# Performance work log

Measured on AMD Instinct MI355X. Metric: run time of the kernel, lower is better.

The kernel has to match this reference:

```python
import jax, jax.numpy as jnp
import numpy as np

DIM = 128; D_STATE = 16; D_CONV = 4; EXPAND = 2
D_INNER = DIM * EXPAND            # 256
DT_RANK = (DIM + 15) // 16        # 8
B, H, W = 2, 56, 56


def _ln(x, w, b):
    m = jnp.mean(x, -1, keepdims=True)
    v = jnp.var(x, -1, keepdims=True)
    return (x - m) * jax.lax.rsqrt(v + 1e-5) * w + b


def _mamba(x, in_w, conv_w, conv_b, xproj_w, dt_w, dt_b, A_log, Dp, out_w):
    # x: (B, L, DIM)
    Bb, L, _ = x.shape
    xz = x @ in_w.T                                   # (B,L,2*D_INNER)
    xi, z = jnp.split(xz, 2, axis=-1)
    # causal depthwise conv1d (pad left d_conv-1, truncate to L)
    xc = jnp.transpose(xi, (0, 2, 1))                 # (B,D_INNER,L)
    xc = jax.lax.conv_general_dilated(
        xc, conv_w, (1,), [(D_CONV - 1, 0)],
        dimension_numbers=('NCH', 'OIH', 'NCH'),
        feature_group_count=D_INNER) + conv_b[None, :, None]
    xs = jax.nn.silu(jnp.transpose(xc, (0, 2, 1)))    # (B,L,D_INNER)
    dbl = xs @ xproj_w.T                              # (B,L,DT_RANK+2*D_STATE)
    dt = jax.nn.softplus(dbl[..., :DT_RANK] @ dt_w.T + dt_b)   # (B,L,D_INNER)
    Bc = dbl[..., DT_RANK:DT_RANK + D_STATE]          # (B,L,D_STATE)
    Cc = dbl[..., DT_RANK + D_STATE:]                 # (B,L,D_STATE)
    A = -jnp.exp(A_log)                               # (D_INNER,D_STATE)
    dA = jnp.exp(dt[..., None] * A)                   # (B,L,D_INNER,D_STATE)
    dBu = (dt * xs)[..., None] * Bc[:, :, None, :]    # (B,L,D_INNER,D_STATE)

    def step(h, inp):
        a, bu, c = inp
        h = a * h + bu                                # (B,D_INNER,D_STATE)
        return h, jnp.einsum('bdn,bn->bd', h, c)

    h0 = jnp.zeros((Bb, D_INNER, D_STATE), x.dtype)
    _, ys = jax.lax.scan(step, h0, (jnp.moveaxis(dA, 1, 0),
                                    jnp.moveaxis(dBu, 1, 0),
                                    jnp.moveaxis(Cc, 1, 0)))
    y = jnp.moveaxis(ys, 0, 1) + xs * Dp              # (B,L,D_INNER)
    y = y * jax.nn.silu(z)
    return y @ out_w.T                                # (B,L,DIM)


def _forward(x, norm_h_w, norm_h_b, norm_v_w, norm_v_b,
             dw_w, dw_b, pw_w, pw_b,
             h_in_w, h_conv_w, h_conv_b, h_xproj_w, h_dt_w, h_dt_b, h_A_log, h_D, h_out_w,
             v_in_w, v_conv_w, v_conv_b, v_xproj_w, v_dt_w, v_dt_b, v_A_log, v_D, v_out_w,
             ca_fc1_w, ca_fc2_w):
    Bb, C, Hh, Ww = x.shape
    # local branch: depthwise 3x3 + GELU + 1x1
    lf = jax.lax.conv_general_dilated(
        x, dw_w, (1, 1), [(1, 1), (1, 1)],
        dimension_numbers=('NCHW', 'OIHW', 'NCHW'),
        feature_group_count=C) + dw_b[None, :, None, None]
    lf = jax.nn.gelu(lf, approximate=False)
    lf = jnp.einsum('bchw,oc->bohw', lf, pw_w[:, :, 0, 0]) + pw_b[None, :, None, None]
    # horizontal scan: row-major tokens
    xh = _ln(x.reshape(Bb, C, Hh * Ww).transpose(0, 2, 1), norm_h_w, norm_h_b)
    oh = _mamba(xh, h_in_w, h_conv_w, h_conv_b, h_xproj_w, h_dt_w, h_dt_b,
                h_A_log, h_D, h_out_w)
    oh = oh.transpose(0, 2, 1).reshape(Bb, C, Hh, Ww)
    # vertical scan: column-major tokens
    xv = _ln(jnp.transpose(x, (0, 1, 3, 2)).reshape(Bb, C, Ww * Hh).transpose(0, 2, 1),
             norm_v_w, norm_v_b)
    ov = _mamba(xv, v_in_w, v_conv_w, v_conv_b, v_xproj_w, v_dt_w, v_dt_b,
                v_A_log, v_D, v_out_w)
    ov = jnp.transpose(ov.transpose(0, 2, 1).reshape(Bb, C, Ww, Hh), (0, 1, 3, 2))
    fused = oh + ov + lf
    # channel attention
    y = jnp.mean(fused, axis=(2, 3))                  # (B,C)
    y = jax.nn.sigmoid(jax.nn.relu(y @ ca_fc1_w.T) @ ca_fc2_w.T)
    return fused * y[:, :, None, None] + x


def setup_inputs() -> dict:
    key = jax.random.key(0)
    ks = iter(jax.random.split(key, 64))
    def nrm(shape, scale):
        return jax.random.normal(next(ks), shape, jnp.float32) * scale
    d = {}
    d['x'] = nrm((B, DIM, H, W), 1.0)
    d['norm_h_w'] = jnp.ones((DIM,), jnp.float32); d['norm_h_b'] = jnp.zeros((DIM,), jnp.float32)
    d['norm_v_w'] = jnp.ones((DIM,), jnp.float32); d['norm_v_b'] = jnp.zeros((DIM,), jnp.float32)
    d['dw_w'] = nrm((DIM, 1, 3, 3), 1.0 / 3.0)
    d['dw_b'] = jnp.zeros((DIM,), jnp.float32)
    d['pw_w'] = nrm((DIM, DIM, 1, 1), DIM ** -0.5)
    d['pw_b'] = jnp.zeros((DIM,), jnp.float32)
    for p in ('h', 'v'):
        d[p + '_in_w'] = nrm((2 * D_INNER, DIM), DIM ** -0.5)
        d[p + '_conv_w'] = nrm((D_INNER, 1, D_CONV), D_CONV ** -0.5)
        d[p + '_conv_b'] = jnp.zeros((D_INNER,), jnp.float32)
        d[p + '_xproj_w'] = nrm((DT_RANK + 2 * D_STATE, D_INNER), D_INNER ** -0.5)
        d[p + '_dt_w'] = nrm((D_INNER, DT_RANK), DT_RANK ** -0.5)
        d[p + '_dt_b'] = jnp.full((D_INNER,), -2.0, jnp.float32)  # small positive dt
        d[p + '_A_log'] = jnp.log(jnp.tile(jnp.arange(1, D_STATE + 1, dtype=jnp.float32), (D_INNER, 1)))
        d[p + '_D'] = jnp.ones((D_INNER,), jnp.float32)
        d[p + '_out_w'] = nrm((DIM, D_INNER), D_INNER ** -0.5)
    d['ca_fc1_w'] = nrm((DIM // 4, DIM), DIM ** -0.5)
    d['ca_fc2_w'] = nrm((DIM, DIM // 4), (DIM // 4) ** -0.5)
    return d


def reference(x, norm_h_w, norm_h_b, norm_v_w, norm_v_b,
              dw_w, dw_b, pw_w, pw_b,
              h_in_w, h_conv_w, h_conv_b, h_xproj_w, h_dt_w, h_dt_b, h_A_log, h_D, h_out_w,
              v_in_w, v_conv_w, v_conv_b, v_xproj_w, v_dt_w, v_dt_b, v_A_log, v_D, v_out_w,
              ca_fc1_w, ca_fc2_w):
    return _forward(x, norm_h_w, norm_h_b, norm_v_w, norm_v_b,
                    dw_w, dw_b, pw_w, pw_b,
                    h_in_w, h_conv_w, h_conv_b, h_xproj_w, h_dt_w, h_dt_b, h_A_log, h_D, h_out_w,
                    v_in_w, v_conv_w, v_conv_b, v_xproj_w, v_dt_w, v_dt_b, v_A_log, v_D, v_out_w,
                    ca_fc1_w, ca_fc2_w)
```

## Files before the change

kernel.cpp:

```cpp
#include <hip/hip_runtime.h>
#include <hip/hip_bf16.h>

typedef __hip_bfloat16 bf16;
__device__ __forceinline__ float b2f(bf16 v){ return __bfloat162float(v); }
__device__ __forceinline__ bf16 f2b(float v){ return __float2bfloat16(v); }

typedef __attribute__((ext_vector_type(8))) short frag_ab;
typedef __attribute__((ext_vector_type(4))) float frag_cd;
typedef __attribute__((ext_vector_type(4))) short short4v;

__device__ __forceinline__ frag_ab ld_frag_2xb64(const bf16* p){
  union { frag_ab f; short4v h[2]; } u;
  u.h[0] = *reinterpret_cast<const short4v*>(p);
  u.h[1] = *reinterpret_cast<const short4v*>(p+4);
  return u.f;
}

__device__ __forceinline__ void st_agent(float* p, float v){
  __hip_atomic_store(p, v, __ATOMIC_RELAXED, __HIP_MEMORY_SCOPE_AGENT);
}
__device__ __forceinline__ float ld_agent(const float* p){
  return __hip_atomic_load(p, __ATOMIC_RELAXED, __HIP_MEMORY_SCOPE_AGENT);
}

#define LLEN 3136
#define BATCH 2
#define NCHUNK 49
#define LC 64

__global__ void k_front(const float* __restrict__ x, const float* __restrict__ dww,
                        const float* __restrict__ dwb, bf16* __restrict__ tmp,
                        const float* nhw_, const float* nhb_, const float* nvw_,
                        const float* nvb_, bf16* __restrict__ xln,
                        float* __restrict__ YMEAN, int* __restrict__ ZCNT){
  int blk = blockIdx.x;
  int tid = threadIdx.x;
  if (blk < 1024){
    int bc = blk & 255;
    int seg = blk >> 8;
    int c = bc & 127;
    if (blk == 0){
      if (tid < 256) YMEAN[tid] = 0.f;
      if (tid < 4)   ZCNT[tid] = 0;
    }
    const float* xp = x + (size_t)bc*LLEN;
    float w[9];
    #pragma unroll
    for (int i=0;i<9;i++) w[i] = dww[c*9+i];
    float bias = dwb[c];
    int pstart = seg * 784;
    for (int p = pstart + tid; p < pstart + 784; p += 256){
      int i = p/56, j = p%56;
      float acc = bias;
      #pragma unroll
      for (int a=0;a<3;a++){
        int ii = i + a - 1;
        if (ii < 0 || ii >= 56) continue;
        #pragma unroll
        for (int bb=0;bb<3;bb++){
          int jj = j + bb - 1;
          if (jj < 0 || jj >= 56) continue;
          acc += w[a*3+bb] * xp[ii*56+jj];
        }
      }
      float g = 0.5f*acc*(1.0f + erff(acc*0.70710678118654752f));
      tmp[(size_t)bc*LLEN + p] = f2b(g);
    }
  } else {
    int idx2 = blk - 1024;
    int h = idx2 % 56, b = idx2 / 56;
    __shared__ float sx[128][57];
    __shared__ float smean[56], srstd[56];
    __shared__ float wh[128], bh[128], wv_[128], bv_[128];
    if (tid < 128){ wh[tid]=nhw_[tid]; bh[tid]=nhb_[tid];
                    wv_[tid]=nvw_[tid]; bv_[tid]=nvb_[tid]; }
    for (int idx = tid; idx < 128*56; idx += 256){
      int c = idx / 56, w = idx % 56;
      sx[c][w] = x[((size_t)(b*128+c))*LLEN + h*56 + w];
    }
    __syncthreads();
    if (tid < 56){
      float s=0.f, s2=0.f;
      for (int c=0;c<128;c++){ float v = sx[c][tid]; s+=v; s2+=v*v; }
      float m = s*(1.f/128.f);
      float var = s2*(1.f/128.f) - m*m;
      smean[tid]=m; srstd[tid]=rsqrtf(var+1e-5f);
    }
    __syncthreads();
    bf16* outh = xln;
    bf16* outv = xln + (size_t)BATCH*LLEN*128;
    for (int idx = tid; idx < 56*128; idx += 256){
      int w = idx >> 7, c = idx & 127;
      float v = (sx[c][w]-smean[w])*srstd[w];
      outh[((size_t)b*LLEN + h*56 + w)*128 + c] = f2b(v*wh[c]+bh[c]);
      outv[((size_t)b*LLEN + w*56 + h)*128 + c] = f2b(v*wv_[c]+bv_[c]);
    }
  }
}

__global__ void k_inproj(const bf16* __restrict__ xln, const float* __restrict__ hw,
                         const float* __restrict__ vw, bf16* __restrict__ XI, bf16* __restrict__ Z){
  int dir = blockIdx.z;
  const bf16* A = xln + (size_t)dir*BATCH*LLEN*128;
  const float* W = dir ? vw : hw;
  int m0 = blockIdx.x*64;
  int npair = blockIdx.y*128;
  __shared__ __align__(16) bf16 sA[64][136];
  __shared__ __align__(16) bf16 sW[64][136];
  int tid = threadIdx.x;
  #pragma unroll
  for (int r=0;r<4;r++){
    int idx = tid + r*256;
    int row = idx >> 4, c8 = (idx & 15)*8;
    *reinterpret_cast<float4*>(&sA[row][c8]) =
        *reinterpret_cast<const float4*>(&A[(size_t)(m0+row)*128 + c8]);
  }
  int wv2 = tid >> 6, lane = tid & 63;
  int qd = lane >> 4, mr = lane & 15;
  bf16* dst = (npair < 256) ? XI : Z;
  int nbase0 = npair & 255;
  size_t dslab = (size_t)dir*BATCH*LLEN*256;
  #pragma unroll
  for (int nt=0; nt<2; nt++){
    int n0 = npair + nt*64;
    __syncthreads();
    #pragma unroll
    for (int r=0;r<8;r++){
      int idx = tid + r*256;
      int row = idx >> 5, c4 = (idx & 31)*4;
      float4 w4 = *reinterpret_cast<const float4*>(&W[(size_t)(n0+row)*128 + c4]);
      bf16 t4[4] = {f2b(w4.x), f2b(w4.y), f2b(w4.z), f2b(w4.w)};
      *reinterpret_cast<double*>(&sW[row][c4]) = *reinterpret_cast<double*>(t4);
    }
    __syncthreads();
    frag_cd acc[4] = {};
    #pragma unroll
    for (int k0=0;k0<128;k0+=32){
      frag_ab af = *reinterpret_cast<frag_ab*>(&sA[wv2*16+mr][k0+qd*8]);
      #pragma unroll
      for (int t=0;t<4;t++){
        frag_ab bfr = *reinterpret_cast<frag_ab*>(&sW[t*16+mr][k0+qd*8]);
        acc[t] = __builtin_amdgcn_mfma_f32_16x16x32_bf16(af, bfr, acc[t], 0, 0, 0);
      }
    }
    int nb = nbase0 + nt*64;
    #pragma unroll
    for (int t=0;t<4;t++)
      #pragma unroll
      for (int r=0;r<4;r++){
        int row = m0 + wv2*16 + qd*4 + r;
        int col = nb + t*16 + mr;
        dst[dslab + (size_t)row*256 + col] = f2b(acc[t][r]);
      }
  }
}

__global__ void k_dbl(const bf16* __restrict__ XI,
                      const float* hcw, const float* hcb, const float* vcw, const float* vcb,
                      const float* __restrict__ hx, const float* __restrict__ vx,
                      const float* hdw, const float* vdw, const float* hdb, const float* vdb,
                      bf16* __restrict__ XS2, bf16* __restrict__ DT2,
                      float* __restrict__ Bf, float* __restrict__ Cf){
  int m0 = blockIdx.x*64;
  int bd = m0 / LLEN;
  int l0m = m0 % LLEN;
  int dirq = bd >> 1;
  const bf16* XId = XI + (size_t)bd*LLEN*256;
  const float* W = dirq ? vx : hx;
  const float* cw = dirq ? vcw : hcw;
  const float* cb = dirq ? vcb : hcb;
  __shared__ __align__(16) bf16 sA[67][264];
  __shared__ __align__(16) bf16 sW[48][264];
  __shared__ float sdbl[64][49];
  int tid = threadIdx.x;
  for (int idx = tid; idx < 67*32; idx += 256){
    int row = idx >> 5, c8 = (idx & 31)*8;
    int l = l0m - 3 + row;
    float4 v = make_float4(0.f,0.f,0.f,0.f);
    if (l >= 0) v = *reinterpret_cast<const float4*>(&XId[(size_t)l*256 + c8]);
    *reinterpret_cast<float4*>(&sA[row][c8]) = v;
  }
  #pragma unroll
  for (int r=0;r<12;r++){
    int idx = tid + r*256;
    int row = idx >> 6, c4 = (idx & 63)*4;
    bf16 t4[4] = {f2b(0.f), f2b(0.f), f2b(0.f), f2b(0.f)};
    if (row < 40){
      float4 w4 = *reinterpret_cast<const float4*>(&W[(size_t)row*256 + c4]);
      t4[0]=f2b(w4.x); t4[1]=f2b(w4.y); t4[2]=f2b(w4.z); t4[3]=f2b(w4.w);
    }
    *reinterpret_cast<double*>(&sW[row][c4]) = *reinterpret_cast<double*>(t4);
  }
  __syncthreads();
  {
    float w0=cw[tid*4], w1=cw[tid*4+1], w2=cw[tid*4+2], w3=cw[tid*4+3];
    float cbias = cb[tid];
    size_t x2base = ((size_t)bd*16 + (tid>>4))*LLEN + l0m;
    int c16 = tid & 15;
    float xm3 = b2f(sA[0][tid]), xm2 = b2f(sA[1][tid]), xm1 = b2f(sA[2][tid]);
    #pragma unroll 4
    for (int j=0;j<64;j++){
      float x0 = b2f(sA[j+3][tid]);
      float acc = cbias + w0*xm3 + w1*xm2 + w2*xm1 + w3*x0;
      float s = acc / (1.f + __expf(-acc));
      bf16 sv = f2b(s);
      sA[j][tid] = sv;
      XS2[(x2base + j)*16 + c16] = sv;
      xm3=xm2; xm2=xm1; xm1=x0;
    }
  }
  __syncthreads();
  int wv2 = tid >> 6, lane = tid & 63;
  int qd = lane >> 4, mr = lane & 15;
  frag_cd acc[3] = {};
  #pragma unroll
  for (int k0=0;k0<256;k0+=32){
    frag_ab af = *reinterpret_cast<frag_ab*>(&sA[wv2*16+mr][k0+qd*8]);
    #pragma unroll
    for (int t=0;t<3;t++){
      frag_ab bfr = *reinterpret_cast<frag_ab*>(&sW[t*16+mr][k0+qd*8]);
      acc[t] = __builtin_amdgcn_mfma_f32_16x16x32_bf16(af, bfr, acc[t], 0, 0, 0);
    }
  }
  #pragma unroll
  for (int t=0;t<3;t++)
    #pragma unroll
    for (int r=0;r<4;r++){
      int col = t*16 + mr;
      if (col < 40) sdbl[wv2*16 + qd*4 + r][col] = acc[t][r];
    }
  __syncthreads();
  const float* dtw = dirq ? vdw : hdw;
  const float* dtb = dirq ? vdb : hdb;
  float w8[8];
  #pragma unroll
  for (int r=0;r<8;r++) w8[r] = dtw[tid*8+r];
  float biasv = dtb[tid];
  size_t d2base = ((size_t)bd*16 + (tid>>4))*LLEN + l0m;
  int c16 = tid & 15;
  for (int row=0; row<64; row++){
    float a = biasv;
    #pragma unroll
    for (int r=0;r<8;r++) a += sdbl[row][r]*w8[r];
    float sv = (a > 20.f) ? a : __logf(1.f + __expf(a));
    DT2[(d2base + row)*16 + c16] = f2b(sv);
  }
  #pragma unroll
  for (int r=0;r<8;r++){
    int idx = tid + r*256;
    int row = idx >> 5, o = idx & 31;
    float v = sdbl[row][8+o];
    size_t rr = (size_t)(m0+row)*16;
    if (o < 16) Bf[rr + o] = v;
    else        Cf[rr + (o-16)] = v;
  }
}

__global__ void k_scan1(const bf16* __restrict__ DT2, const bf16* __restrict__ XS2,
                        const float* __restrict__ Bc, const float* hA, const float* vA,
                        float* __restrict__ Pbuf, float* __restrict__ Hbuf){
  int bd = blockIdx.z;
  int g  = blockIdx.y;
  int ck = blockIdx.x;
  int l0 = ck*LC;
  const float* Bd = Bc + (size_t)bd*LLEN*16;
  const float* Alog = (bd >> 1) ? vA : hA;
  int tid = threadIdx.x;
  int dl = tid >> 4, n = tid & 15;
  float A = -__expf(Alog[(g*16+dl)*16+n]);
  __shared__ float sdt[LC][16], sxs[LC][16], sB[LC][16];
  size_t base2 = (((size_t)bd*16 + g)*LLEN + l0)*16;
  #pragma unroll
  for (int r=0;r<4;r++){
    int idx = tid + r*256;
    sdt[idx>>4][idx&15] = b2f(DT2[base2 + idx]);
    sxs[idx>>4][idx&15] = b2f(XS2[base2 + idx]);
    (&sB[0][0])[idx] = Bd[(size_t)l0*16 + idx];
  }
  __syncthreads();
  float h = 0.f, P = 1.f;
  #pragma unroll 8
  for (int i=0;i<LC;i++){
    float a = sdt[i][dl];
    float u = sxs[i][dl];
    float dA = __expf(a * A);
    h = dA*h + (a*u)*sB[i][n];
    P *= dA;
  }
  size_t sidx = (((size_t)bd*16 + g)*NCHUNK + ck)*256 + tid;
  Pbuf[sidx] = P;
  Hbuf[sidx] = h;
}

__global__ void k_scan2(const float* __restrict__ Pbuf, float* __restrict__ Hbuf){
  int q = blockIdx.x;
  int tid = threadIdx.x;
  size_t qb = (size_t)q*NCHUNK*256 + tid;
  float Pv[7], Hv[7];
  float carry = 0.f;
  #pragma unroll
  for (int j=0;j<7;j++){
    Pv[j] = Pbuf[qb + (size_t)j*256];
    Hv[j] = Hbuf[qb + (size_t)j*256];
  }
  #pragma unroll
  for (int b=0;b<7;b++){
    float Pn[7], Hn[7];
    if (b < 6){
      #pragma unroll
      for (int j=0;j<7;j++){
        Pn[j] = Pbuf[qb + (size_t)((b+1)*7+j)*256];
        Hn[j] = Hbuf[qb + (size_t)((b+1)*7+j)*256];
      }
    }
    #pragma unroll
    for (int j=0;j<7;j++){
      Hbuf[qb + (size_t)(b*7+j)*256] = carry;
      carry = Pv[j]*carry + Hv[j];
    }
    if (b < 6){
      #pragma unroll
      for (int j=0;j<7;j++){ Pv[j] = Pn[j]; Hv[j] = Hn[j]; }
    }
  }
}

__global__ void k_scan3(const bf16* __restrict__ DT2, const bf16* __restrict__ XS2,
                        const float* __restrict__ Bc, const float* __restrict__ Cc,
                        const float* hA, const float* vA,
                        const float* __restrict__ Hbuf, bf16* __restrict__ ys){
  int bd = blockIdx.z;
  int g  = blockIdx.y;
  int ck = blockIdx.x;
  int l0 = ck*LC;
  const float* Bd = Bc + (size_t)bd*LLEN*16;
  const float* Cd = Cc + (size_t)bd*LLEN*16;
  bf16* yd = ys + (size_t)bd*LLEN*256;
  const float* Alog = (bd >> 1) ? vA : hA;
  int tid = threadIdx.x;
  int dl = tid >> 4, n = tid & 15;
  float A = -__expf(Alog[(g*16+dl)*16+n]);
  __shared__ float sdt[LC][16], sxs[LC][16], sB[LC][16], sC[LC][16];
  __shared__ float sp2[16][272];
  size_t base2 = (((size_t)bd*16 + g)*LLEN + l0)*16;
  #pragma unroll
  for (int r=0;r<4;r++){
    int idx = tid + r*256;
    sdt[idx>>4][idx&15] = b2f(DT2[base2 + idx]);
    sxs[idx>>4][idx&15] = b2f(XS2[base2 + idx]);
    (&sB[0][0])[idx] = Bd[(size_t)l0*16 + idx];
    (&sC[0][0])[idx] = Cd[(size_t)l0*16 + idx];
  }
  size_t sidx = (((size_t)bd*16 + g)*NCHUNK + ck)*256 + tid;
  float h = Hbuf[sidx];
  __syncthreads();
  int swz = dl*17 + n;
  int i_local = tid >> 4;
  int c16 = tid & 15;
  int rbase = c16*17;
  for (int i0=0; i0<LC; i0+=16){
    #pragma unroll
    for (int ii=0;ii<16;ii++){
      int i = i0 + ii;
      float a = sdt[i][dl];
      float u = sxs[i][dl];
      float dA = __expf(a * A);
      h = dA*h + (a*u)*sB[i][n];
      sp2[ii][swz] = h * sC[i][n];
    }
    __syncthreads();
    const float* row = &sp2[i_local][rbase];
    float s = 0.f;
    #pragma unroll
    for (int k=0;k<16;k++) s += row[k];
    yd[(size_t)(l0+i0+i_local)*256 + g*16 + c16] = f2b(s);
    __syncthreads();
  }
}

__global__ void k_outgemm(const bf16* __restrict__ ys, const bf16* __restrict__ XS2,
                          const bf16* __restrict__ Z, const float* __restrict__ hD,
                          const float* __restrict__ vD, const float* __restrict__ how,
                          const float* __restrict__ vow, bf16* __restrict__ OD){
  int dir = blockIdx.y;
  size_t slab = (size_t)dir*BATCH*LLEN*256;
  const float* W = dir ? vow : how;
  const float* Dw = dir ? vD : hD;
  bf16* od = OD + (size_t)dir*BATCH*LLEN*128;
  int m0 = blockIdx.x*32;
  int bd = dir*2 + m0/LLEN;
  int lbase = m0 % LLEN;
  __shared__ __align__(16) bf16 sA[32][264];
  __shared__ __align__(16) bf16 sW[64][264];
  int tid = threadIdx.x;
  #pragma unroll
  for (int r=0;r<4;r++){
    int idx = tid + r*256;
    int row = idx >> 5, c8 = (idx & 31)*8;
    size_t e = slab + (size_t)(m0+row)*256 + c8;
    size_t e2 = (((size_t)bd*16 + (c8>>4))*LLEN + lbase + row)*16 + (c8&15);
    bf16 yb[8], xb[8], zb[8], ob[8];
    *reinterpret_cast<float4*>(yb) = *reinterpret_cast<const float4*>(&ys[e]);
    *reinterpret_cast<float4*>(xb) = *reinterpret_cast<const float4*>(&XS2[e2]);
    *reinterpret_cast<float4*>(zb) = *reinterpret_cast<const float4*>(&Z[e]);
    #pragma unroll
    for (int j=0;j<8;j++){
      float Dv = Dw[c8 + j];
      float yv = b2f(yb[j]) + b2f(xb[j])*Dv;
      float zv = b2f(zb[j]);
      ob[j] = f2b(yv * (zv/(1.f+__expf(-zv))));
    }
    *reinterpret_cast<float4*>(&sA[row][c8]) = *reinterpret_cast<float4*>(ob);
  }
  int wv2 = tid >> 6, lane = tid & 63;
  int qd = lane >> 4, mr = lane & 15;
  int msub = wv2 & 1, tpair = (wv2 >> 1)*2;
  #pragma unroll
  for (int nh=0; nh<2; nh++){
    int n0 = nh*64;
    __syncthreads();
    #pragma unroll
    for (int r=0;r<16;r++){
      int idx = tid + r*256;
      int row = idx >> 6, c4 = (idx & 63)*4;
      float4 w4 = *reinterpret_cast<const float4*>(&W[(size_t)(n0+row)*256 + c4]);
      bf16 t4[4] = {f2b(w4.x), f2b(w4.y), f2b(w4.z), f2b(w4.w)};
      *reinterpret_cast<double*>(&sW[row][c4]) = *reinterpret_cast<double*>(t4);
    }
    __syncthreads();
    frag_cd acc[2] = {};
    #pragma unroll
    for (int k0=0;k0<256;k0+=32){
      frag_ab af = *reinterpret_cast<frag_ab*>(&sA[msub*16+mr][k0+qd*8]);
      #pragma unroll
      for (int i=0;i<2;i++){
        frag_ab bfr = *reinterpret_cast<frag_ab*>(&sW[(tpair+i)*16+mr][k0+qd*8]);
        acc[i] = __builtin_amdgcn_mfma_f32_16x16x32_bf16(af, bfr, acc[i], 0, 0, 0);
      }
    }
    #pragma unroll
    for (int i=0;i<2;i++)
      #pragma unroll
      for (int r=0;r<4;r++){
        int row = m0 + msub*16 + qd*4 + r;
        int col = n0 + (tpair+i)*16 + mr;
        od[(size_t)row*128 + col] = f2b(acc[i][r]);
      }
  }
}

__global__ void k_pwcomb(const bf16* __restrict__ tmp, const float* __restrict__ pww,
                         const float* __restrict__ pwb, const bf16* __restrict__ OD,
                         const float* __restrict__ x, float* __restrict__ out,
                         float* __restrict__ YMEAN, int* __restrict__ CNTPW,
                         int* __restrict__ FLAG, float* __restrict__ GATE,
                         const float* __restrict__ fc1, const float* __restrict__ fc2){
  int p0 = blockIdx.x * 64;
  int m0 = blockIdx.y * 64;
  int b  = blockIdx.z;
  const bf16* T = tmp + (size_t)b*128*LLEN;
  const bf16* od0 = OD + (size_t)b*LLEN*128;
  const bf16* od1 = OD + (size_t)(BATCH + b)*LLEN*128;
  __shared__ __align__(16) bf16 sA[64][136];
  __shared__ __align__(16) bf16 sBt[64][132];
  __shared__ float sOD[64][65];
  __shared__ float ym[128], s1g[32];
  __shared__ int slast;
  int tid = threadIdx.x;
  #pragma unroll
  for (int r=0;r<8;r++){
    int idx = tid + r*256;
    int row = idx >> 5, c4 = (idx & 31)*4;
    float4 w4 = *reinterpret_cast<const float4*>(&pww[(size_t)(m0+row)*128 + c4]);
    bf16 t4[4] = {f2b(w4.x), f2b(w4.y), f2b(w4.z), f2b(w4.w)};
    *reinterpret_cast<double*>(&sA[row][c4]) = *reinterpret_cast<double*>(t4);
  }
  #pragma unroll
  for (int r=0;r<8;r++){
    int idx = tid + r*256;
    int c = idx >> 4, p4 = (idx & 15)*4;
    union { double d; bf16 v[4]; } u;
    u.d = *reinterpret_cast<const double*>(&T[(size_t)c*LLEN + p0 + p4]);
    #pragma unroll
    for (int j=0;j<4;j++) sBt[p4+j][c] = u.v[j];
  }
  #pragma unroll
  for (int r=0;r<8;r++){
    int idx = tid + r*256;
    int prow = idx >> 5, mp = (idx & 31)*2;
    int p = p0 + prow;
    int pi = p/56, pj = p%56;
    int pt = pj*56 + pi;
    bf16 a0[2], a1[2];
    *reinterpret_cast<float*>(a0) = *reinterpret_cast<const float*>(&od0[(size_t)p*128 + m0 + mp]);
    *reinterpret_cast<float*>(a1) = *reinterpret_cast<const float*>(&od1[(size_t)pt*128 + m0 + mp]);
    sOD[prow][mp]   = b2f(a0[0]) + b2f(a1[0]);
    sOD[prow][mp+1] = b2f(a0[1]) + b2f(a1[1]);
  }
  __syncthreads();
  int wv2 = tid >> 6, lane = tid & 63;
  int qd = lane >> 4, mr = lane & 15;
  frag_cd acc[4] = {};
  #pragma unroll
  for (int k0=0;k0<128;k0+=32){
    frag_ab af = *reinterpret_cast<frag_ab*>(&sA[wv2*16+mr][k0+qd*8]);
    #pragma unroll
    for (int t=0;t<4;t++){
      frag_ab bfr = ld_frag_2xb64(&sBt[t*16+mr][k0+qd*8]);
      acc[t] = __builtin_amdgcn_mfma_f32_16x16x32_bf16(af, bfr, acc[t], 0, 0, 0);
    }
  }
  float vals[4][4];
  #pragma unroll
  for (int r=0;r<4;r++){
    int m = m0 + wv2*16 + qd*4 + r;
    float bias = pwb[m];
    float s = 0.f;
    #pragma unroll
    for (int t=0;t<4;t++){
      float val = acc[t][r] + bias + sOD[t*16+mr][m - m0];
      vals[t][r] = val;
      s += val;
    }
    s += __shfl_xor(s, 1, 16);
    s += __shfl_xor(s, 2, 16);
    s += __shfl_xor(s, 4, 16);
    s += __shfl_xor(s, 8, 16);
    if (mr == 0) atomicAdd(&YMEAN[b*128 + m], s);
  }
  __syncthreads();
  if (tid == 0) slast = (atomicAdd(&CNTPW[b], 1) == 2*49 - 1);
  __syncthreads();
  if (slast){
    if (tid < 128)
      ym[tid] = ld_agent(&YMEAN[b*128+tid]) * (1.f/(float)LLEN);
    __syncthreads();
    {
      int o = tid >> 3, part = tid & 7;
      float a = 0.f;
      #pragma unroll
      for (int k=0;k<16;k++) a += ym[part*16 + k] * fc1[o*128 + part*16 + k];
      a += __shfl_xor(a, 1, 8);
      a += __shfl_xor(a, 2, 8);
      a += __shfl_xor(a, 4, 8);
      if (part == 0) s1g[o] = fmaxf(a, 0.f);
    }
    __syncthreads();
    if (tid < 128){
      float a = 0.f;
      #pragma unroll
      for (int j=0;j<32;j++) a += s1g[j]*fc2[tid*32+j];
      st_agent(&GATE[b*128+tid], 1.f/(1.f+__expf(-a)));
    }
    __syncthreads();
    if (tid == 0)
      __hip_atomic_store(&FLAG[b], 1, __ATOMIC_RELEASE, __HIP_MEMORY_SCOPE_AGENT);
  } else {
    if (tid == 0)
      while (__hip_atomic_load(&FLAG[b], __ATOMIC_ACQUIRE, __HIP_MEMORY_SCOPE_AGENT) == 0)
        __builtin_amdgcn_s_sleep(2);
  }
  __syncthreads();
  float g4[4];
  #pragma unroll
  for (int r=0;r<4;r++){
    int m = m0 + wv2*16 + qd*4 + r;
    g4[r] = ld_agent(&GATE[b*128+m]);
  }
  #pragma unroll
  for (int t=0;t<4;t++)
    #pragma unroll
    for (int r=0;r<4;r++){
      int m = m0 + wv2*16 + qd*4 + r;
      int p = p0 + t*16 + mr;
      size_t i = ((size_t)b*128 + m)*LLEN + p;
      out[i] = vals[t][r]*g4[r] + x[i];
    }
}

extern "C" void kernel_launch(void* const* d_in, const int* in_sizes, int n_in,
                              void* d_out, int out_size, void* d_ws, size_t ws_size,
                              hipStream_t stream) {
  const float* x      = (const float*)d_in[0];
  const float* nhw    = (const float*)d_in[1];
  const float* nhb    = (const float*)d_in[2];
  const float* nvw    = (const float*)d_in[3];
  const float* nvb    = (const float*)d_in[4];
  const float* dww    = (const float*)d_in[5];
  const float* dwb    = (const float*)d_in[6];
  const float* pww    = (const float*)d_in[7];
  const float* pwb    = (const float*)d_in[8];
  const float* h_inw  = (const float*)d_in[9];
  const float* h_cw   = (const float*)d_in[10];
  const float* h_cb   = (const float*)d_in[11];
  const float* h_xw   = (const float*)d_in[12];
  const float* h_dtw  = (const float*)d_in[13];
  const float* h_dtb  = (const float*)d_in[14];
  const float* h_Al   = (const float*)d_in[15];
  const float* h_D    = (const float*)d_in[16];
  const float* h_ow   = (const float*)d_in[17];
  const float* v_inw  = (const float*)d_in[18];
  const float* v_cw   = (const float*)d_in[19];
  const float* v_cb   = (const float*)d_in[20];
  const float* v_xw   = (const float*)d_in[21];
  const float* v_dtw  = (const float*)d_in[22];
  const float* v_dtb  = (const float*)d_in[23];
  const float* v_Al   = (const float*)d_in[24];
  const float* v_D    = (const float*)d_in[25];
  const float* v_ow   = (const float*)d_in[26];
  const float* fc1    = (const float*)d_in[27];
  const float* fc2    = (const float*)d_in[28];

  float* out = (float*)d_out;

  char* base = (char*)d_ws;
  bf16*  XLN   = (bf16*)(base + 1605632);
  bf16*  DT2   = (bf16*)(base + 0);
  bf16*  OD    = (bf16*)(base + 0);
  bf16*  XI    = (bf16*)(base + 6422528);
  bf16*  YS    = (bf16*)(base + 6422528);
  bf16*  Z     = (bf16*)(base + 12845056);
  bf16*  XS2   = (bf16*)(base + 19267584);
  float* Bf    = (float*)(base + 25690112);
  float* Cf    = (float*)(base + 26492928);
  float* Hbuf  = (float*)(base + 27295744);
  float* YMEAN = (float*)(base + 30507008);
  bf16*  TMP   = (bf16*)(base + 30508032);
  float* Pbuf  = (float*)(base + 32113664);
  int*   ZCNT  = (int*)  (base + 35324928);
  float* GATE  = (float*)(base + 35325440);
  int*   CNTPW = ZCNT;
  int*   FLAG  = ZCNT + 2;

  k_front<<<dim3(1024 + 56*BATCH), dim3(256), 0, stream>>>(x, dww, dwb, TMP,
                                                           nhw, nhb, nvw, nvb, XLN, YMEAN, ZCNT);
  k_inproj<<<dim3(98,4,2), dim3(256), 0, stream>>>(XLN, h_inw, v_inw, XI, Z);
  k_dbl<<<dim3(196), dim3(256), 0, stream>>>(XI, h_cw, h_cb, v_cw, v_cb,
                                             h_xw, v_xw, h_dtw, v_dtw, h_dtb, v_dtb,
                                             XS2, DT2, Bf, Cf);
  k_scan1<<<dim3(NCHUNK,16,4), dim3(256), 0, stream>>>(DT2, XS2, Bf, h_Al, v_Al, Pbuf, Hbuf);
  k_scan2<<<dim3(64), dim3(256), 0, stream>>>(Pbuf, Hbuf);
  k_scan3<<<dim3(NCHUNK,16,4), dim3(256), 0, stream>>>(DT2, XS2, Bf, Cf, h_Al, v_Al, Hbuf, YS);
  k_outgemm<<<dim3(196,2), dim3(256), 0, stream>>>(YS, XS2, Z, h_D, v_D, h_ow, v_ow, OD);
  k_pwcomb<<<dim3(49,2,BATCH), dim3(256), 0, stream>>>(TMP, pww, pwb, OD, x, out,
                                                       YMEAN, CNTPW, FLAG, GATE, fc1, fc2);
}
```

Baseline: 223.2 us.

## Pre-convert weights to bf16 once in front kernel; stage depthwise conv input in LDS

Adds 64 extra blocks to the front kernel that convert the in-proj, x-proj, out-proj and pointwise weights from fp32 to bf16 once. Downstream GEMM kernels then load bf16 weights with 16-byte vector loads instead of converting fp32 per block. It also stages the depthwise-conv input rows in shared memory with zero padding, which removes the per-tap bounds checks. The risk is that some bf16 weight buffers live in the output buffer as scratch, so pwcomb writes to the output must not overlap reads of WBIN, WBOUT and WBX.

```diff
diff --git a/kernel.cpp b/kernel.cpp
--- a/kernel.cpp
+++ b/kernel.cpp
@@ -32,7 +32,13 @@
                         const float* __restrict__ dwb, bf16* __restrict__ tmp,
                         const float* nhw_, const float* nhb_, const float* nvw_,
                         const float* nvb_, bf16* __restrict__ xln,
-                        float* __restrict__ YMEAN, int* __restrict__ ZCNT){
+                        float* __restrict__ YMEAN, int* __restrict__ ZCNT,
+                        const float* __restrict__ h_inw, const float* __restrict__ v_inw,
+                        const float* __restrict__ h_ow,  const float* __restrict__ v_ow,
+                        const float* __restrict__ pww,   const float* __restrict__ h_xw,
+                        const float* __restrict__ v_xw,
+                        bf16* __restrict__ WBIN, bf16* __restrict__ WBOUT,
+                        bf16* __restrict__ WBPW, bf16* __restrict__ WBX){
   int blk = blockIdx.x;
   int tid = threadIdx.x;
   if (blk < 1024){
@@ -44,29 +50,33 @@
       if (tid < 4)   ZCNT[tid] = 0;
     }
     const float* xp = x + (size_t)bc*LLEN;
+    __shared__ float sxr[16][60];
+    int r0 = seg*14;
+    for (int idx = tid; idx < 16*56; idx += 256){
+      int rr = idx/56, cc = idx%56;
+      int gr = r0 - 1 + rr;
+      sxr[rr][cc+1] = (gr >= 0 && gr < 56) ? xp[gr*56+cc] : 0.f;
+    }
+    if (tid < 16){ sxr[tid][0] = 0.f; sxr[tid][57] = 0.f; }
     float w[9];
     #pragma unroll
     for (int i=0;i<9;i++) w[i] = dww[c*9+i];
     float bias = dwb[c];
+    __syncthreads();
     int pstart = seg * 784;
     for (int p = pstart + tid; p < pstart + 784; p += 256){
       int i = p/56, j = p%56;
+      int li = i - r0;
       float acc = bias;
       #pragma unroll
-      for (int a=0;a<3;a++){
-        int ii = i + a - 1;
-        if (ii < 0 || ii >= 56) continue;
+      for (int a=0;a<3;a++)
         #pragma unroll
-        for (int bb=0;bb<3;bb++){
-          int jj = j + bb - 1;
-          if (jj < 0 || jj >= 56) continue;
-          acc += w[a*3+bb] * xp[ii*56+jj];
-        }
-      }
+        for (int bb=0;bb<3;bb++)
+          acc += w[a*3+bb] * sxr[li+a][j+bb];
       float g = 0.5f*acc*(1.0f + erff(acc*0.70710678118654752f));
       tmp[(size_t)bc*LLEN + p] = f2b(g);
     }
-  } else {
+  } else if (blk < 1136){
     int idx2 = blk - 1024;
     int h = idx2 % 56, b = idx2 / 56;
     __shared__ float sx[128][57];
@@ -95,14 +105,70 @@
       outh[((size_t)b*LLEN + h*56 + w)*128 + c] = f2b(v*wh[c]+bh[c]);
       outv[((size_t)b*LLEN + w*56 + h)*128 + c] = f2b(v*wv_[c]+bv_[c]);
     }
-  }
-}
-
-__global__ void k_inproj(const bf16* __restrict__ xln, const float* __restrict__ hw,
-                         const float* __restrict__ vw, bf16* __restrict__ XI, bf16* __restrict__ Z){
+  } else {
+    int pblk = blk - 1136;
+    int t16 = tid*16;
+    if (pblk < 32){
+      int g = pblk*4096 + t16;
+      int dir = g >> 16, off = g & 65535;
+      const float* src = (dir ? v_inw : h_inw) + off;
+      bf16* dst = WBIN + g;
+      #pragma unroll
+      for (int r=0;r<4;r++){
+        float4 w4 = *reinterpret_cast<const float4*>(src + r*4);
+        bf16 t4[4] = {f2b(w4.x), f2b(w4.y), f2b(w4.z), f2b(w4.w)};
+        *reinterpret_cast<double*>(dst + r*4) = *reinterpret_cast<double*>(t4);
+      }
+    } else if (pblk < 48){
+      int g = (pblk-32)*4096 + t16;
+      int dir = g >> 15, off = g & 32767;
+      const float* src = (dir ? v_ow : h_ow) + off;
+      bf16* dst = WBOUT + g;
+      #pragma unroll
+      for (int r=0;r<4;r++){
+        float4 w4 = *reinterpret_cast<const float4*>(src + r*4);
+        bf16 t4[4] = {f2b(w4.x), f2b(w4.y), f2b(w4.z), f2b(w4.w)};
+        *reinterpret_cast<double*>(dst + r*4) = *reinterpret_cast<double*>(t4);
+      }
+    } else if (pblk < 52){
+      int g = (pblk-48)*4096 + t16;
+      const float* src = pww + g;
+      bf16* dst = WBPW + g;
+      #pragma unroll
+      for (int r=0;r<4;r++){
+        float4 w4 = *reinterpret_cast<const float4*>(src + r*4);
+        bf16 t4[4] = {f2b(w4.x), f2b(w4.y), f2b(w4.z), f2b(w4.w)};
+        *reinterpret_cast<double*>(dst + r*4) = *reinterpret_cast<double*>(t4);
+      }
+    } else if (pblk < 58){
+      int g = (pblk-52)*4096 + t16;
+      int dir = (g >= 12288) ? 1 : 0;
+      int off = g - dir*12288;
+      int rr = off >> 8, cc = off & 255;
+      bf16* dst = WBX + g;
+      if (rr < 40){
+        const float* src = (dir ? v_xw : h_xw) + rr*256 + cc;
+        #pragma unroll
+        for (int r=0;r<4;r++){
+          float4 w4 = *reinterpret_cast<const float4*>(src + r*4);
+          bf16 t4[4] = {f2b(w4.x), f2b(w4.y), f2b(w4.z), f2b(w4.w)};
+          *reinterpret_cast<double*>(dst + r*4) = *reinterpret_cast<double*>(t4);
+        }
+      } else {
+        bf16 z4[4] = {f2b(0.f), f2b(0.f), f2b(0.f), f2b(0.f)};
+        double zd = *reinterpret_cast<double*>(z4);
+        #pragma unroll
+        for (int r=0;r<4;r++) *reinterpret_cast<double*>(dst + r*4) = zd;
+      }
+    }
+  }
+}
+
+__global__ void k_inproj(const bf16* __restrict__ xln, const bf16* __restrict__ WBIN,
+                         bf16* __restrict__ XI, bf16* __restrict__ Z){
   int dir = blockIdx.z;
   const bf16* A = xln + (size_t)dir*BATCH*LLEN*128;
-  const float* W = dir ? vw : hw;
+  const bf16* Wb = WBIN + (size_t)dir*512*128;
   int m0 = blockIdx.x*64;
   int npair = blockIdx.y*128;
   __shared__ __align__(16) bf16 sA[64][136];
@@ -125,12 +191,11 @@
     int n0 = npair + nt*64;
     __syncthreads();
     #pragma unroll
-    for (int r=0;r<8;r++){
+    for (int r=0;r<4;r++){
       int idx = tid + r*256;
-      int row = idx >> 5, c4 = (idx & 31)*4;
-      float4 w4 = *reinterpret_cast<const float4*>(&W[(size_t)(n0+row)*128 + c4]);
-      bf16 t4[4] = {f2b(w4.x), f2b(w4.y), f2b(w4.z), f2b(w4.w)};
-      *reinterpret_cast<double*>(&sW[row][c4]) = *reinterpret_cast<double*>(t4);
+      int row = idx >> 4, c8 = (idx & 15)*8;
+      *reinterpret_cast<float4*>(&sW[row][c8]) =
+          *reinterpret_cast<const float4*>(&Wb[(size_t)(n0+row)*128 + c8]);
     }
     __syncthreads();
     frag_cd acc[4] = {};
@@ -157,7 +222,7 @@
 
 __global__ void k_dbl(const bf16* __restrict__ XI,
                       const float* hcw, const float* hcb, const float* vcw, const float* vcb,
-                      const float* __restrict__ hx, const float* __restrict__ vx,
+                      const bf16* __restrict__ WBX,
                       const float* hdw, const float* vdw, const float* hdb, const float* vdb,
                       bf16* __restrict__ XS2, bf16* __restrict__ DT2,
                       float* __restrict__ Bf, float* __restrict__ Cf){
@@ -166,7 +231,7 @@
   int l0m = m0 % LLEN;
   int dirq = bd >> 1;
   const bf16* XId = XI + (size_t)bd*LLEN*256;
-  const float* W = dirq ? vx : hx;
+  const bf16* Wb = WBX + (size_t)dirq*48*256;
   const float* cw = dirq ? vcw : hcw;
   const float* cb = dirq ? vcb : hcb;
   __shared__ __align__(16) bf16 sA[67][264];
@@ -181,15 +246,11 @@
     *reinterpret_cast<float4*>(&sA[row][c8]) = v;
   }
   #pragma unroll
-  for (int r=0;r<12;r++){
-    int idx = tid + r*256;
-    int row = idx >> 6, c4 = (idx & 63)*4;
-    bf16 t4[4] = {f2b(0.f), f2b(0.f), f2b(0.f), f2b(0.f)};
-    if (row < 40){
-      float4 w4 = *reinterpret_cast<const float4*>(&W[(size_t)row*256 + c4]);
-      t4[0]=f2b(w4.x); t4[1]=f2b(w4.y); t4[2]=f2b(w4.z); t4[3]=f2b(w4.w);
-    }
-    *reinterpret_cast<double*>(&sW[row][c4]) = *reinterpret_cast<double*>(t4);
+  for (int r=0;r<6;r++){
+    int idx = tid + r*256;
+    int row = idx >> 5, c8 = (idx & 31)*8;
+    *reinterpret_cast<float4*>(&sW[row][c8]) =
+        *reinterpret_cast<const float4*>(&Wb[(size_t)row*256 + c8]);
   }
   __syncthreads();
   {
@@ -380,11 +441,11 @@
 
 __global__ void k_outgemm(const bf16* __restrict__ ys, const bf16* __restrict__ XS2,
                           const bf16* __restrict__ Z, const float* __restrict__ hD,
-                          const float* __restrict__ vD, const float* __restrict__ how,
-                          const float* __restrict__ vow, bf16* __restrict__ OD){
+                          const float* __restrict__ vD, const bf16* __restrict__ WBOUT,
+                          bf16* __restrict__ OD){
   int dir = blockIdx.y;
   size_t slab = (size_t)dir*BATCH*LLEN*256;
-  const float* W = dir ? vow : how;
+  const bf16* Wb = WBOUT + (size_t)dir*128*256;
   const float* Dw = dir ? vD : hD;
   bf16* od = OD + (size_t)dir*BATCH*LLEN*128;
   int m0 = blockIdx.x*32;
@@ -420,12 +481,11 @@
     int n0 = nh*64;
     __syncthreads();
     #pragma unroll
-    for (int r=0;r<16;r++){
+    for (int r=0;r<8;r++){
       int idx = tid + r*256;
-      int row = idx >> 6, c4 = (idx & 63)*4;
-      float4 w4 = *reinterpret_cast<const float4*>(&W[(size_t)(n0+row)*256 + c4]);
-      bf16 t4[4] = {f2b(w4.x), f2b(w4.y), f2b(w4.z), f2b(w4.w)};
-      *reinterpret_cast<double*>(&sW[row][c4]) = *reinterpret_cast<double*>(t4);
+      int row = idx >> 5, c8 = (idx & 31)*8;
+      *reinterpret_cast<float4*>(&sW[row][c8]) =
+          *reinterpret_cast<const float4*>(&Wb[(size_t)(n0+row)*256 + c8]);
     }
     __syncthreads();
     frag_cd acc[2] = {};
@@ -449,7 +509,7 @@
   }
 }
 
-__global__ void k_pwcomb(const bf16* __restrict__ tmp, const float* __restrict__ pww,
+__global__ void k_pwcomb(const bf16* __restrict__ tmp, const bf16* __restrict__ WBPW,
                          const float* __restrict__ pwb, const bf16* __restrict__ OD,
                          const float* __restrict__ x, float* __restrict__ out,
                          float* __restrict__ YMEAN, int* __restrict__ CNTPW,
@@ -468,12 +528,11 @@
   __shared__ int slast;
   int tid = threadIdx.x;
   #pragma unroll
-  for (int r=0;r<8;r++){
-    int idx = tid + r*256;
-    int row = idx >> 5, c4 = (idx & 31)*4;
-    float4 w4 = *reinterpret_cast<const float4*>(&pww[(size_t)(m0+row)*128 + c4]);
-    bf16 t4[4] = {f2b(w4.x), f2b(w4.y), f2b(w4.z), f2b(w4.w)};
-    *reinterpret_cast<double*>(&sA[row][c4]) = *reinterpret_cast<double*>(t4);
+  for (int r=0;r<4;r++){
+    int idx = tid + r*256;
+    int row = idx >> 4, c8 = (idx & 15)*8;
+    *reinterpret_cast<float4*>(&sA[row][c8]) =
+        *reinterpret_cast<const float4*>(&WBPW[(size_t)(m0+row)*128 + c8]);
   }
   #pragma unroll
   for (int r=0;r<8;r++){
@@ -613,6 +672,10 @@
 
   float* out = (float*)d_out;
 
+  bf16* WBIN  = (bf16*)((char*)d_out + 0);
+  bf16* WBOUT = (bf16*)((char*)d_out + 262144);
+  bf16* WBX   = (bf16*)((char*)d_out + 393216);
+
   char* base = (char*)d_ws;
   bf16*  XLN   = (bf16*)(base + 1605632);
   bf16*  DT2   = (bf16*)(base + 0);
@@ -629,19 +692,21 @@
   float* Pbuf  = (float*)(base + 32113664);
   int*   ZCNT  = (int*)  (base + 35324928);
   float* GATE  = (float*)(base + 35325440);
+  bf16*  WBPW  = (bf16*) (base + 35326464);
   int*   CNTPW = ZCNT;
   int*   FLAG  = ZCNT + 2;
 
-  k_front<<<dim3(1024 + 56*BATCH), dim3(256), 0, stream>>>(x, dww, dwb, TMP,
-                                                           nhw, nhb, nvw, nvb, XLN, YMEAN, ZCNT);
-  k_inproj<<<dim3(98,4,2), dim3(256), 0, stream>>>(XLN, h_inw, v_inw, XI, Z);
+  k_front<<<dim3(1024 + 56*BATCH + 64), dim3(256), 0, stream>>>(
+      x, dww, dwb, TMP, nhw, nhb, nvw, nvb, XLN, YMEAN, ZCNT,
+      h_inw, v_inw, h_ow, v_ow, pww, h_xw, v_xw, WBIN, WBOUT, WBPW, WBX);
+  k_inproj<<<dim3(98,4,2), dim3(256), 0, stream>>>(XLN, WBIN, XI, Z);
   k_dbl<<<dim3(196), dim3(256), 0, stream>>>(XI, h_cw, h_cb, v_cw, v_cb,
-                                             h_xw, v_xw, h_dtw, v_dtw, h_dtb, v_dtb,
+                                             WBX, h_dtw, v_dtw, h_dtb, v_dtb,
                                              XS2, DT2, Bf, Cf);
   k_scan1<<<dim3(NCHUNK,16,4), dim3(256), 0, stream>>>(DT2, XS2, Bf, h_Al, v_Al, Pbuf, Hbuf);
   k_scan2<<<dim3(64), dim3(256), 0, stream>>>(Pbuf, Hbuf);
   k_scan3<<<dim3(NCHUNK,16,4), dim3(256), 0, stream>>>(DT2, XS2, Bf, Cf, h_Al, v_Al, Hbuf, YS);
-  k_outgemm<<<dim3(196,2), dim3(256), 0, stream>>>(YS, XS2, Z, h_D, v_D, h_ow, v_ow, OD);
-  k_pwcomb<<<dim3(49,2,BATCH), dim3(256), 0, stream>>>(TMP, pww, pwb, OD, x, out,
+  k_outgemm<<<dim3(196,2), dim3(256), 0, stream>>>(YS, XS2, Z, h_D, v_D, WBOUT, OD);
+  k_pwcomb<<<dim3(49,2,BATCH), dim3(256), 0, stream>>>(TMP, WBPW, pwb, OD, x, out,
                                                        YMEAN, CNTPW, FLAG, GATE, fc1, fc2);
 }
```

Result: no change. 220.4 us (-1.3%).
